# Kernel tuning notes

Measured on AMD Instinct MI355X. Metric: run time of the kernel, lower is better.

The kernel has to match this reference:

```python
import jax, jax.numpy as jnp
import numpy as np

NUM_HEADS = 8
DIM_HIDDEN = 512


def setup_inputs() -> dict:
    key = jax.random.key(0)
    k1, k2, k3, k4 = jax.random.split(key, 4)
    B, N, C = 4, 2048, DIM_HIDDEN
    x = jax.random.normal(k1, (B, N, C), dtype=jnp.float32)
    # proj_in: Linear(C, 3C, bias=False); stored as [in, out] for x @ W
    W_in = jax.random.normal(k2, (C, 3 * C), dtype=jnp.float32) * (1.0 / np.sqrt(C))
    # proj_out: Linear(C, C) with bias
    W_out = jax.random.normal(k3, (C, C), dtype=jnp.float32) * (1.0 / np.sqrt(C))
    b_out = jax.random.normal(k4, (C,), dtype=jnp.float32) * 0.01
    return {"x": x, "W_in": W_in, "W_out": W_out, "b_out": b_out}


def reference(x, W_in, W_out, b_out):
    B, N, C = x.shape
    H = NUM_HEADS
    D = C // H
    scale = D ** -0.5
    qkv = (x @ W_in).reshape(B, N, 3, H, D)
    qkv = jnp.transpose(qkv, (2, 0, 3, 1, 4))  # [3, B, H, N, D]
    q, k, v = qkv[0], qkv[1], qkv[2]
    attn = jnp.einsum("bhqd,bhkd->bhqk", q, k) * scale
    attn = jax.nn.softmax(attn, axis=-1)
    out = jnp.einsum("bhqk,bhkd->bhqd", attn, v)  # [B, H, N, D]
    out = jnp.transpose(out, (0, 2, 1, 3)).reshape(B, N, C)
    return out @ W_out + b_out
```

## Files before the change

### kernel.cpp

```cpp
#include <hip/hip_runtime.h>

typedef unsigned short u16;
typedef unsigned int   u32;
using s16x8 = __attribute__((ext_vector_type(8))) short;
using s16x4 = __attribute__((ext_vector_type(4))) short;
using f32x4 = __attribute__((ext_vector_type(4))) float;

#define NB   4
#define SEQ  2048
#define CH   512
#define NH   8
#define HD   64
#define C3   1536
#define LOG2E 1.44269504088896f

__device__ __forceinline__ u16 f2bf(float f) {
  u32 u = __float_as_uint(f);
  u32 r = u + 0x7fffu + ((u >> 16) & 1u);
  return (u16)(r >> 16);
}

__device__ __forceinline__ u32 cvtpk(float a, float b) {
  u32 r;
  asm("v_cvt_pk_bf16_f32 %0, %1, %2" : "=v"(r) : "v"(a), "v"(b));
  return r;
}

__device__ __forceinline__ float ex2(float x) {
#if __has_builtin(__builtin_amdgcn_exp2f)
  return __builtin_amdgcn_exp2f(x);
#else
  return exp2f(x);
#endif
}

#define GLL16(gp, lp) __builtin_amdgcn_global_load_lds( \
    (const __attribute__((address_space(1))) u32*)(gp), \
    (__attribute__((address_space(3))) u32*)(lp), 16, 0, 0)

__global__ __launch_bounds__(256) void conv_x(const float* __restrict__ in,
                                              u16* __restrict__ out, int n4) {
  int i = blockIdx.x * 256 + threadIdx.x;
  if (i >= n4) return;
  float4 v = ((const float4*)in)[i];
  u32 a = (u32)f2bf(v.x) | ((u32)f2bf(v.y) << 16);
  u32 b = (u32)f2bf(v.z) | ((u32)f2bf(v.w) << 16);
  ((uint2*)out)[i] = make_uint2(a, b);
}

__global__ __launch_bounds__(256) void conv_tr(const float* __restrict__ in,
                                               u16* __restrict__ out, int R, int C) {
  __shared__ float tb[64][68];
  const int c0 = blockIdx.x * 64, r0 = blockIdx.y * 64;
  const int t = threadIdx.x;
#pragma unroll
  for (int i = 0; i < 4; ++i) {
    int idx = i * 1024 + t * 4;
    int r = idx >> 6, c = idx & 63;
    float4 v = *(const float4*)(&in[(size_t)(r0 + r) * C + c0 + c]);
    tb[r][c] = v.x; tb[r][c + 1] = v.y; tb[r][c + 2] = v.z; tb[r][c + 3] = v.w;
  }
  __syncthreads();
  const int cc = t >> 2, rr0 = (t & 3) * 16;
  u16 tmp[16];
#pragma unroll
  for (int j = 0; j < 16; ++j) tmp[j] = f2bf(tb[rr0 + j][cc]);
#pragma unroll
  for (int j = 0; j < 4; ++j) {
    u32 a = (u32)tmp[4 * j] | ((u32)tmp[4 * j + 1] << 16);
    u32 b = (u32)tmp[4 * j + 2] | ((u32)tmp[4 * j + 3] << 16);
    *(uint2*)(&out[(size_t)(c0 + cc) * R + r0 + rr0 + 4 * j]) = make_uint2(a, b);
  }
}

template <int KTOT>
__device__ __forceinline__ void gemm_core(const u16* __restrict__ Ag,
                                          const u16* __restrict__ Bg,
                                          int m0, int n0, f32x4 (&acc)[4][4],
                                          u16* As, u16* Bs) {
  const int t = threadIdx.x;
  const int l = t & 63, w = t >> 6;
  const int wr = w >> 1, wc = w & 1;
  const int lo = l & 15, hi = l >> 4;
  const int srow_base = w * 8 + (l >> 3);
  const int scolb = (l & 7) * 16;

  for (int k0 = 0; k0 < KTOT; k0 += 64) {
    __syncthreads();
#pragma unroll
    for (int i = 0; i < 4; ++i) {
      int row = i * 32 + srow_base;
      int sw  = (row & 7) << 4;
      GLL16((const char*)Ag + (size_t)(m0 + row) * 1024 + k0 * 2 + (scolb ^ sw),
            (char*)As + row * 128 + scolb);
      GLL16((const char*)Bg + (size_t)(n0 + row) * 1024 + k0 * 2 + (scolb ^ sw),
            (char*)Bs + row * 128 + scolb);
    }
    __syncthreads();
#pragma unroll
    for (int s = 0; s < 2; ++s) {
      s16x8 af[4], bf[4];
#pragma unroll
      for (int mi = 0; mi < 4; ++mi) {
        int row = wr * 64 + mi * 16 + lo;
        af[mi] = *(const s16x8*)((const char*)As + row * 128 +
                                 ((s * 64 + hi * 16) ^ ((row & 7) << 4)));
      }
#pragma unroll
      for (int ni = 0; ni < 4; ++ni) {
        int row = wc * 64 + ni * 16 + lo;
        bf[ni] = *(const s16x8*)((const char*)Bs + row * 128 +
                                 ((s * 64 + hi * 16) ^ ((row & 7) << 4)));
      }
#pragma unroll
      for (int mi = 0; mi < 4; ++mi)
#pragma unroll
        for (int ni = 0; ni < 4; ++ni)
          acc[mi][ni] = __builtin_amdgcn_mfma_f32_16x16x32_bf16(af[mi], bf[ni],
                                                                acc[mi][ni], 0, 0, 0);
    }
  }
}

__global__ __launch_bounds__(256) void gemm_qkv(const u16* __restrict__ xb,
                                                const u16* __restrict__ WinT,
                                                u16* __restrict__ qb,
                                                u16* __restrict__ kb,
                                                u16* __restrict__ vb) {
  __shared__ __align__(16) u16 As[8192];
  __shared__ __align__(16) u16 Bs[8192];
  const int m0 = blockIdx.y * 128, n0 = blockIdx.x * 128;
  f32x4 acc[4][4];
#pragma unroll
  for (int i = 0; i < 4; ++i)
#pragma unroll
    for (int j = 0; j < 4; ++j) acc[i][j] = (f32x4){0.f, 0.f, 0.f, 0.f};

  gemm_core<CH>(xb, WinT, m0, n0, acc, As, Bs);

  const int t = threadIdx.x, l = t & 63, w = t >> 6;
  const int wr = w >> 1, wc = w & 1, lo = l & 15, hi = l >> 4;
#pragma unroll
  for (int ni = 0; ni < 4; ++ni) {
    const int n = n0 + wc * 64 + ni * 16 + lo;
    const int tq = n >> 9, h = (n >> 6) & 7, d = n & 63;
    u16* dst = (tq == 0) ? qb : ((tq == 1) ? kb : vb);
    const float sc = (tq == 0) ? 0.125f * LOG2E : 1.0f;
#pragma unroll
    for (int mi = 0; mi < 4; ++mi)
#pragma unroll
      for (int r = 0; r < 4; ++r) {
        const int m = m0 + wr * 64 + mi * 16 + hi * 4 + r;
        const int b = m >> 11, ns = m & (SEQ - 1);
        dst[((size_t)((b * NH + h) * SEQ + ns)) * HD + d] = f2bf(acc[mi][ni][r] * sc);
      }
  }
}

__global__ __launch_bounds__(512) void attn(const u16* __restrict__ qg,
                                            const u16* __restrict__ kg,
                                            const u16* __restrict__ vg,
                                            u16* __restrict__ ao) {
  __shared__ __align__(16) u16 Ks[2][4096];
  __shared__ __align__(16) u16 Vs[2][4096];
  __shared__ __align__(16) u16 Ps[8192];
  const int t = threadIdx.x, l = t & 63, w = t >> 6;
  const int lo = l & 15, hi = l >> 4;
  const int wg = blockIdx.x;
  const int L  = (wg & 7) * 64 + (wg >> 3);
  const int bh = L >> 4, qblk = L & 15;
  const int q0 = qblk * 128;
  const u16* qp = qg + (size_t)bh * SEQ * HD;
  const u16* kp = kg + (size_t)bh * SEQ * HD;
  const u16* vp = vg + (size_t)bh * SEQ * HD;

  s16x8 qf[2];
#pragma unroll
  for (int s = 0; s < 2; ++s)
    qf[s] = *(const s16x8*)(qp + (size_t)(q0 + w * 16 + lo) * HD + s * 32 + hi * 8);

  f32x4 oacc[4];
#pragma unroll
  for (int i = 0; i < 4; ++i) oacc[i] = (f32x4){0.f, 0.f, 0.f, 0.f};
  float m_s = -1e30f, l_s = 0.f;

  u16* Pw = Ps + w * 1024;
  const int vkv = (t & 31) * 2, vd0 = (t >> 5) * 4;
  const int ksrc = (t >> 3) * 128 + (((t & 7) * 16) ^ (((t >> 3) & 7) << 4));
  const int swl = (lo & 7) << 4;

  GLL16((const char*)kp + ksrc, (char*)&Ks[0][0] + t * 16);
  s16x4 vr0 = *(const s16x4*)(vp + (size_t)vkv * HD + vd0);
  s16x4 vr1 = *(const s16x4*)(vp + (size_t)(vkv + 1) * HD + vd0);
#pragma unroll
  for (int j = 0; j < 4; ++j) {
    int d = vd0 + j;
    u32 pw = (u32)(u16)vr0[j] | ((u32)(u16)vr1[j] << 16);
    *(u32*)((char*)&Vs[0][0] + ((d * 128 + vkv * 2) ^ ((d & 7) << 4))) = pw;
  }
  __syncthreads();

  for (int it = 0; it < 32; ++it) {
    const int cur = it & 1, nxt = cur ^ 1;
    const u16* Kc = &Ks[cur][0];
    const u16* Vc = &Vs[cur][0];
    if (it < 31) {
      const size_t nb = (size_t)(it + 1) * 64;
      GLL16((const char*)(kp + nb * HD) + ksrc, (char*)&Ks[nxt][0] + t * 16);
      vr0 = *(const s16x4*)(vp + (nb + vkv) * HD + vd0);
      vr1 = *(const s16x4*)(vp + (nb + vkv + 1) * HD + vd0);
    }

    f32x4 st[4];
#pragma unroll
    for (int i = 0; i < 4; ++i) st[i] = (f32x4){0.f, 0.f, 0.f, 0.f};
    __builtin_amdgcn_s_setprio(1);
#pragma unroll
    for (int s = 0; s < 2; ++s)
#pragma unroll
      for (int ct = 0; ct < 4; ++ct) {
        int row = ct * 16 + lo;
        s16x8 kf = *(const s16x8*)((const char*)Kc + row * 128 +
                                   ((s * 64 + hi * 16) ^ ((row & 7) << 4)));
        st[ct] = __builtin_amdgcn_mfma_f32_16x16x32_bf16(kf, qf[s], st[ct], 0, 0, 0);
      }
    __builtin_amdgcn_s_setprio(0);

    float a0 = fmaxf(fmaxf(st[0][0], st[1][0]), fmaxf(st[2][0], st[3][0]));
    float a1 = fmaxf(fmaxf(st[0][1], st[1][1]), fmaxf(st[2][1], st[3][1]));
    float a2 = fmaxf(fmaxf(st[0][2], st[1][2]), fmaxf(st[2][2], st[3][2]));
    float a3 = fmaxf(fmaxf(st[0][3], st[1][3]), fmaxf(st[2][3], st[3][3]));
    float mx = fmaxf(fmaxf(a0, a1), fmaxf(a2, a3));
    mx = fmaxf(mx, __shfl_xor(mx, 16));
    mx = fmaxf(mx, __shfl_xor(mx, 32));
    if (__any(mx > m_s + 8.0f)) {
      const float mn = fmaxf(m_s, mx);
      const float rs = ex2(m_s - mn);
      m_s = mn;
      l_s *= rs;
#pragma unroll
      for (int ct = 0; ct < 4; ++ct) {
        oacc[ct][0] *= rs; oacc[ct][1] *= rs;
        oacc[ct][2] *= rs; oacc[ct][3] *= rs;
      }
    }
    float psum[4];
#pragma unroll
    for (int ct = 0; ct < 4; ++ct) {
      float p0 = ex2(st[ct][0] - m_s), p1 = ex2(st[ct][1] - m_s);
      float p2 = ex2(st[ct][2] - m_s), p3 = ex2(st[ct][3] - m_s);
      st[ct][0] = p0; st[ct][1] = p1; st[ct][2] = p2; st[ct][3] = p3;
      psum[ct] = (p0 + p1) + (p2 + p3);
    }
    float sum = (psum[0] + psum[1]) + (psum[2] + psum[3]);
    sum += __shfl_xor(sum, 16);
    sum += __shfl_xor(sum, 32);
    l_s += sum;

#pragma unroll
    for (int ct = 0; ct < 4; ++ct) {
      u32 pk0 = cvtpk(st[ct][0], st[ct][1]);
      u32 pk1 = cvtpk(st[ct][2], st[ct][3]);
      *(uint2*)((char*)Pw + ((lo * 128 + ct * 32 + hi * 8) ^ swl)) =
          make_uint2(pk0, pk1);
    }

    s16x8 pf[2];
#pragma unroll
    for (int s = 0; s < 2; ++s)
      pf[s] = *(const s16x8*)((const char*)Pw + ((lo * 128 + s * 64 + hi * 16) ^ swl));
    __builtin_amdgcn_s_setprio(1);
#pragma unroll
    for (int s = 0; s < 2; ++s)
#pragma unroll
      for (int ct = 0; ct < 4; ++ct) {
        int row = ct * 16 + lo;
        s16x8 vt = *(const s16x8*)((const char*)Vc + row * 128 +
                                   ((s * 64 + hi * 16) ^ ((row & 7) << 4)));
        oacc[ct] = __builtin_amdgcn_mfma_f32_16x16x32_bf16(vt, pf[s], oacc[ct], 0, 0, 0);
      }
    __builtin_amdgcn_s_setprio(0);

    if (it < 31) {
#pragma unroll
      for (int j = 0; j < 4; ++j) {
        int d = vd0 + j;
        u32 pw = (u32)(u16)vr0[j] | ((u32)(u16)vr1[j] << 16);
        *(u32*)((char*)&Vs[nxt][0] + ((d * 128 + vkv * 2) ^ ((d & 7) << 4))) = pw;
      }
      asm volatile("s_waitcnt vmcnt(0) lgkmcnt(0)" ::: "memory");
      __builtin_amdgcn_s_barrier();
      __builtin_amdgcn_sched_barrier(0);
    }
  }

  const int b = bh >> 3, h = bh & 7;
  const float inv = 1.0f / l_s;
  u16* aop = ao + ((size_t)(b * SEQ) + q0 + w * 16 + lo) * CH + h * HD;
#pragma unroll
  for (int ct = 0; ct < 4; ++ct) {
    u32 o0 = cvtpk(oacc[ct][0] * inv, oacc[ct][1] * inv);
    u32 o1 = cvtpk(oacc[ct][2] * inv, oacc[ct][3] * inv);
    *(uint2*)(aop + ct * 16 + hi * 4) = make_uint2(o0, o1);
  }
}

__global__ __launch_bounds__(256) void gemm_out(const u16* __restrict__ ao,
                                                const u16* __restrict__ WoutT,
                                                const float* __restrict__ bias,
                                                float* __restrict__ out) {
  __shared__ __align__(16) u16 As[8192];
  __shared__ __align__(16) u16 Bs[8192];
  const int m0 = blockIdx.y * 128, n0 = blockIdx.x * 128;
  f32x4 acc[4][4];
#pragma unroll
  for (int i = 0; i < 4; ++i)
#pragma unroll
    for (int j = 0; j < 4; ++j) acc[i][j] = (f32x4){0.f, 0.f, 0.f, 0.f};

  gemm_core<CH>(ao, WoutT, m0, n0, acc, As, Bs);

  const int t = threadIdx.x, l = t & 63, w = t >> 6;
  const int wr = w >> 1, wc = w & 1, lo = l & 15, hi = l >> 4;
#pragma unroll
  for (int ni = 0; ni < 4; ++ni) {
    const int n = n0 + wc * 64 + ni * 16 + lo;
    const float bv = bias[n];
#pragma unroll
    for (int mi = 0; mi < 4; ++mi)
#pragma unroll
      for (int r = 0; r < 4; ++r) {
        const int m = m0 + wr * 64 + mi * 16 + hi * 4 + r;
        out[(size_t)m * CH + n] = acc[mi][ni][r] + bv;
      }
  }
}

extern "C" void kernel_launch(void* const* d_in, const int* in_sizes, int n_in,
                              void* d_out, int out_size, void* d_ws, size_t ws_size,
                              hipStream_t stream) {
  const float* x    = (const float*)d_in[0];
  const float* Win  = (const float*)d_in[1];
  const float* Wout = (const float*)d_in[2];
  const float* bout = (const float*)d_in[3];
  float* out = (float*)d_out;
  char* ws = (char*)d_ws;

  const size_t MB = 1u << 20;
  u16* xb    = (u16*)(ws);
  u16* WinT  = (u16*)(ws + 8 * MB);
  u16* WoutT = (u16*)(ws + 10 * MB);
  u16* qb    = (u16*)(ws + 12 * MB);
  u16* kb    = (u16*)(ws + 20 * MB);
  u16* vb    = (u16*)(ws + 28 * MB);
  u16* ao    = (u16*)(ws + 36 * MB);

  conv_x<<<4096, 256, 0, stream>>>(x, xb, (NB * SEQ * CH) / 4);
  conv_tr<<<dim3(C3 / 64, CH / 64), 256, 0, stream>>>(Win, WinT, CH, C3);
  conv_tr<<<dim3(CH / 64, CH / 64), 256, 0, stream>>>(Wout, WoutT, CH, CH);

  gemm_qkv<<<dim3(C3 / 128, (NB * SEQ) / 128), 256, 0, stream>>>(xb, WinT, qb, kb, vb);
  attn<<<512, 512, 0, stream>>>(qb, kb, vb, ao);
  gemm_out<<<dim3(CH / 128, (NB * SEQ) / 128), 256, 0, stream>>>(ao, WoutT, bout, out);
}
```

Before: 109.6 us.

## Process two query tiles per wave in attention to reuse K/V fragments

Attention blocks drop from 8 waves to 4, and each wave now handles 32 query rows as two 16-row groups. Each K and V fragment read from LDS feeds two MFMAs, halving LDS fragment traffic per query row. Each thread now loads twice as much K/V per stage. The lazy rescale threshold branch is removed and the running max is always rescaled. Per-wave register use roughly doubles (two sets of accumulators and scores), and there are fewer waves per block to hide latency.

```diff
diff --git a/kernel.cpp b/kernel.cpp
--- a/kernel.cpp
+++ b/kernel.cpp
@@ -157,7 +157,7 @@
   }
 }
 
-__global__ __launch_bounds__(512) void attn(const u16* __restrict__ qg,
+__global__ __launch_bounds__(256) void attn(const u16* __restrict__ qg_,
                                             const u16* __restrict__ kg,
                                             const u16* __restrict__ vg,
                                             u16* __restrict__ ao) {
@@ -170,30 +170,41 @@
   const int L  = (wg & 7) * 64 + (wg >> 3);
   const int bh = L >> 4, qblk = L & 15;
   const int q0 = qblk * 128;
-  const u16* qp = qg + (size_t)bh * SEQ * HD;
+  const u16* qp = qg_ + (size_t)bh * SEQ * HD;
   const u16* kp = kg + (size_t)bh * SEQ * HD;
   const u16* vp = vg + (size_t)bh * SEQ * HD;
 
-  s16x8 qf[2];
-#pragma unroll
-  for (int s = 0; s < 2; ++s)
-    qf[s] = *(const s16x8*)(qp + (size_t)(q0 + w * 16 + lo) * HD + s * 32 + hi * 8);
-
-  f32x4 oacc[4];
-#pragma unroll
-  for (int i = 0; i < 4; ++i) oacc[i] = (f32x4){0.f, 0.f, 0.f, 0.f};
-  float m_s = -1e30f, l_s = 0.f;
-
-  u16* Pw = Ps + w * 1024;
-  const int vkv = (t & 31) * 2, vd0 = (t >> 5) * 4;
-  const int ksrc = (t >> 3) * 128 + (((t & 7) * 16) ^ (((t >> 3) & 7) << 4));
+  s16x8 qf[2][2];
+#pragma unroll
+  for (int qg = 0; qg < 2; ++qg)
+#pragma unroll
+    for (int s = 0; s < 2; ++s)
+      qf[qg][s] = *(const s16x8*)(qp + (size_t)(q0 + w * 32 + qg * 16 + lo) * HD +
+                                  s * 32 + hi * 8);
+
+  f32x4 oacc[2][4];
+#pragma unroll
+  for (int qg = 0; qg < 2; ++qg)
+#pragma unroll
+    for (int i = 0; i < 4; ++i) oacc[qg][i] = (f32x4){0.f, 0.f, 0.f, 0.f};
+  float m_s[2] = {-1e30f, -1e30f}, l_s[2] = {0.f, 0.f};
+
+  const int vkv = (t & 31) * 2, vd0 = (t >> 5) * 8;
   const int swl = (lo & 7) << 4;
-
-  GLL16((const char*)kp + ksrc, (char*)&Ks[0][0] + t * 16);
-  s16x4 vr0 = *(const s16x4*)(vp + (size_t)vkv * HD + vd0);
-  s16x4 vr1 = *(const s16x4*)(vp + (size_t)(vkv + 1) * HD + vd0);
-#pragma unroll
-  for (int j = 0; j < 4; ++j) {
+  int ksrc[2];
+#pragma unroll
+  for (int i = 0; i < 2; ++i) {
+    int row = i * 32 + (t >> 3);
+    ksrc[i] = row * 128 + (((t & 7) * 16) ^ ((row & 7) << 4));
+  }
+
+#pragma unroll
+  for (int i = 0; i < 2; ++i)
+    GLL16((const char*)kp + ksrc[i], (char*)&Ks[0][0] + i * 4096 + t * 16);
+  s16x8 vr0 = *(const s16x8*)(vp + (size_t)vkv * HD + vd0);
+  s16x8 vr1 = *(const s16x8*)(vp + (size_t)(vkv + 1) * HD + vd0);
+#pragma unroll
+  for (int j = 0; j < 8; ++j) {
     int d = vd0 + j;
     u32 pw = (u32)(u16)vr0[j] | ((u32)(u16)vr1[j] << 16);
     *(u32*)((char*)&Vs[0][0] + ((d * 128 + vkv * 2) ^ ((d & 7) << 4))) = pw;
@@ -206,14 +217,19 @@
     const u16* Vc = &Vs[cur][0];
     if (it < 31) {
       const size_t nb = (size_t)(it + 1) * 64;
-      GLL16((const char*)(kp + nb * HD) + ksrc, (char*)&Ks[nxt][0] + t * 16);
-      vr0 = *(const s16x4*)(vp + (nb + vkv) * HD + vd0);
-      vr1 = *(const s16x4*)(vp + (nb + vkv + 1) * HD + vd0);
-    }
-
-    f32x4 st[4];
-#pragma unroll
-    for (int i = 0; i < 4; ++i) st[i] = (f32x4){0.f, 0.f, 0.f, 0.f};
+#pragma unroll
+      for (int i = 0; i < 2; ++i)
+        GLL16((const char*)(kp + nb * HD) + ksrc[i],
+              (char*)&Ks[nxt][0] + i * 4096 + t * 16);
+      vr0 = *(const s16x8*)(vp + (nb + vkv) * HD + vd0);
+      vr1 = *(const s16x8*)(vp + (nb + vkv + 1) * HD + vd0);
+    }
+
+    f32x4 st[2][4];
+#pragma unroll
+    for (int qg = 0; qg < 2; ++qg)
+#pragma unroll
+      for (int i = 0; i < 4; ++i) st[qg][i] = (f32x4){0.f, 0.f, 0.f, 0.f};
     __builtin_amdgcn_s_setprio(1);
 #pragma unroll
     for (int s = 0; s < 2; ++s)
@@ -222,68 +238,72 @@
         int row = ct * 16 + lo;
         s16x8 kf = *(const s16x8*)((const char*)Kc + row * 128 +
                                    ((s * 64 + hi * 16) ^ ((row & 7) << 4)));
-        st[ct] = __builtin_amdgcn_mfma_f32_16x16x32_bf16(kf, qf[s], st[ct], 0, 0, 0);
+#pragma unroll
+        for (int qg = 0; qg < 2; ++qg)
+          st[qg][ct] = __builtin_amdgcn_mfma_f32_16x16x32_bf16(kf, qf[qg][s],
+                                                               st[qg][ct], 0, 0, 0);
       }
     __builtin_amdgcn_s_setprio(0);
 
-    float a0 = fmaxf(fmaxf(st[0][0], st[1][0]), fmaxf(st[2][0], st[3][0]));
-    float a1 = fmaxf(fmaxf(st[0][1], st[1][1]), fmaxf(st[2][1], st[3][1]));
-    float a2 = fmaxf(fmaxf(st[0][2], st[1][2]), fmaxf(st[2][2], st[3][2]));
-    float a3 = fmaxf(fmaxf(st[0][3], st[1][3]), fmaxf(st[2][3], st[3][3]));
-    float mx = fmaxf(fmaxf(a0, a1), fmaxf(a2, a3));
-    mx = fmaxf(mx, __shfl_xor(mx, 16));
-    mx = fmaxf(mx, __shfl_xor(mx, 32));
-    if (__any(mx > m_s + 8.0f)) {
-      const float mn = fmaxf(m_s, mx);
-      const float rs = ex2(m_s - mn);
-      m_s = mn;
-      l_s *= rs;
+#pragma unroll
+    for (int qg = 0; qg < 2; ++qg) {
+      float a0 = fmaxf(fmaxf(st[qg][0][0], st[qg][1][0]), fmaxf(st[qg][2][0], st[qg][3][0]));
+      float a1 = fmaxf(fmaxf(st[qg][0][1], st[qg][1][1]), fmaxf(st[qg][2][1], st[qg][3][1]));
+      float a2 = fmaxf(fmaxf(st[qg][0][2], st[qg][1][2]), fmaxf(st[qg][2][2], st[qg][3][2]));
+      float a3 = fmaxf(fmaxf(st[qg][0][3], st[qg][1][3]), fmaxf(st[qg][2][3], st[qg][3][3]));
+      float mx = fmaxf(fmaxf(a0, a1), fmaxf(a2, a3));
+      mx = fmaxf(mx, __shfl_xor(mx, 16));
+      mx = fmaxf(mx, __shfl_xor(mx, 32));
+      const float mn = fmaxf(m_s[qg], mx);
+      const float rs = ex2(m_s[qg] - mn);
+      m_s[qg] = mn;
+      const int rb = (w * 32 + qg * 16 + lo) * 128;
+      float sum = 0.f;
 #pragma unroll
       for (int ct = 0; ct < 4; ++ct) {
-        oacc[ct][0] *= rs; oacc[ct][1] *= rs;
-        oacc[ct][2] *= rs; oacc[ct][3] *= rs;
-      }
-    }
-    float psum[4];
-#pragma unroll
-    for (int ct = 0; ct < 4; ++ct) {
-      float p0 = ex2(st[ct][0] - m_s), p1 = ex2(st[ct][1] - m_s);
-      float p2 = ex2(st[ct][2] - m_s), p3 = ex2(st[ct][3] - m_s);
-      st[ct][0] = p0; st[ct][1] = p1; st[ct][2] = p2; st[ct][3] = p3;
-      psum[ct] = (p0 + p1) + (p2 + p3);
-    }
-    float sum = (psum[0] + psum[1]) + (psum[2] + psum[3]);
-    sum += __shfl_xor(sum, 16);
-    sum += __shfl_xor(sum, 32);
-    l_s += sum;
-
-#pragma unroll
-    for (int ct = 0; ct < 4; ++ct) {
-      u32 pk0 = cvtpk(st[ct][0], st[ct][1]);
-      u32 pk1 = cvtpk(st[ct][2], st[ct][3]);
-      *(uint2*)((char*)Pw + ((lo * 128 + ct * 32 + hi * 8) ^ swl)) =
-          make_uint2(pk0, pk1);
-    }
-
-    s16x8 pf[2];
-#pragma unroll
-    for (int s = 0; s < 2; ++s)
-      pf[s] = *(const s16x8*)((const char*)Pw + ((lo * 128 + s * 64 + hi * 16) ^ swl));
+        float p0 = ex2(st[qg][ct][0] - mn), p1 = ex2(st[qg][ct][1] - mn);
+        float p2 = ex2(st[qg][ct][2] - mn), p3 = ex2(st[qg][ct][3] - mn);
+        sum += (p0 + p1) + (p2 + p3);
+        u32 pk0 = cvtpk(p0, p1);
+        u32 pk1 = cvtpk(p2, p3);
+        *(uint2*)((char*)Ps + ((rb + ct * 32 + hi * 8) ^ swl)) = make_uint2(pk0, pk1);
+      }
+      sum += __shfl_xor(sum, 16);
+      sum += __shfl_xor(sum, 32);
+      l_s[qg] = l_s[qg] * rs + sum;
+#pragma unroll
+      for (int ct = 0; ct < 4; ++ct) {
+        oacc[qg][ct][0] *= rs; oacc[qg][ct][1] *= rs;
+        oacc[qg][ct][2] *= rs; oacc[qg][ct][3] *= rs;
+      }
+    }
+
+    s16x8 pf[2][2];
+#pragma unroll
+    for (int qg = 0; qg < 2; ++qg)
+#pragma unroll
+      for (int s = 0; s < 2; ++s)
+        pf[qg][s] = *(const s16x8*)((const char*)Ps +
+                    (((w * 32 + qg * 16 + lo) * 128 + s * 64 + hi * 16) ^ swl));
     __builtin_amdgcn_s_setprio(1);
 #pragma unroll
-    for (int s = 0; s < 2; ++s)
+    for (int s = 0; s < 2; ++s) {
 #pragma unroll
       for (int ct = 0; ct < 4; ++ct) {
         int row = ct * 16 + lo;
         s16x8 vt = *(const s16x8*)((const char*)Vc + row * 128 +
                                    ((s * 64 + hi * 16) ^ ((row & 7) << 4)));
-        oacc[ct] = __builtin_amdgcn_mfma_f32_16x16x32_bf16(vt, pf[s], oacc[ct], 0, 0, 0);
-      }
+#pragma unroll
+        for (int qg = 0; qg < 2; ++qg)
+          oacc[qg][ct] = __builtin_amdgcn_mfma_f32_16x16x32_bf16(vt, pf[qg][s],
+                                                                 oacc[qg][ct], 0, 0, 0);
+      }
+    }
     __builtin_amdgcn_s_setprio(0);
 
     if (it < 31) {
 #pragma unroll
-      for (int j = 0; j < 4; ++j) {
+      for (int j = 0; j < 8; ++j) {
         int d = vd0 + j;
         u32 pw = (u32)(u16)vr0[j] | ((u32)(u16)vr1[j] << 16);
         *(u32*)((char*)&Vs[nxt][0] + ((d * 128 + vkv * 2) ^ ((d & 7) << 4))) = pw;
@@ -295,13 +315,16 @@
   }
 
   const int b = bh >> 3, h = bh & 7;
-  const float inv = 1.0f / l_s;
-  u16* aop = ao + ((size_t)(b * SEQ) + q0 + w * 16 + lo) * CH + h * HD;
-#pragma unroll
-  for (int ct = 0; ct < 4; ++ct) {
-    u32 o0 = cvtpk(oacc[ct][0] * inv, oacc[ct][1] * inv);
-    u32 o1 = cvtpk(oacc[ct][2] * inv, oacc[ct][3] * inv);
-    *(uint2*)(aop + ct * 16 + hi * 4) = make_uint2(o0, o1);
+#pragma unroll
+  for (int qg = 0; qg < 2; ++qg) {
+    const float inv = 1.0f / l_s[qg];
+    u16* aop = ao + ((size_t)(b * SEQ) + q0 + w * 32 + qg * 16 + lo) * CH + h * HD;
+#pragma unroll
+    for (int ct = 0; ct < 4; ++ct) {
+      u32 o0 = cvtpk(oacc[qg][ct][0] * inv, oacc[qg][ct][1] * inv);
+      u32 o1 = cvtpk(oacc[qg][ct][2] * inv, oacc[qg][ct][3] * inv);
+      *(uint2*)(aop + ct * 16 + hi * 4) = make_uint2(o0, o1);
+    }
   }
 }
 
@@ -360,6 +383,6 @@
   conv_tr<<<dim3(CH / 64, CH / 64), 256, 0, stream>>>(Wout, WoutT, CH, CH);
 
   gemm_qkv<<<dim3(C3 / 128, (NB * SEQ) / 128), 256, 0, stream>>>(xb, WinT, qb, kb, vb);
-  attn<<<512, 512, 0, stream>>>(qb, kb, vb, ao);
+  attn<<<512, 256, 0, stream>>>(qb, kb, vb, ao);
   gemm_out<<<dim3(CH / 128, (NB * SEQ) / 128), 256, 0, stream>>>(ao, WoutT, bout, out);
 }
```

Result: slower. 123.8 us (+12.9%).
